# Kernel tuning notes

Measured on AMD Instinct MI355X. Metric: run time of the kernel, lower is better.

The kernel has to match this reference:

```python
import jax, jax.numpy as jnp
import numpy as np

B, NF, EMB = 2048, 32, 64
FEAT_MAP_DIM = [128, 128, 128]  # split_half=True, activation=None


def setup_inputs() -> dict:
    key = jax.random.key(0)
    ks = jax.random.split(key, 7)
    inp = jax.random.normal(ks[0], (B, NF, EMB), dtype=jnp.float32)
    # conv1d_i: in_channels = H_{i-1} * NF, out_channels = FEAT_MAP_DIM[i]
    # H_0 = NF = 32; H_1 = H_2 = 128 // 2 = 64 (split_half)
    in_chs = [NF * NF, (FEAT_MAP_DIM[0] // 2) * NF, (FEAT_MAP_DIM[1] // 2) * NF]
    params = {}
    for i, (ic, oc) in enumerate(zip(in_chs, FEAT_MAP_DIM)):
        bound = 1.0 / np.sqrt(ic)  # torch Conv1d default init range
        params[f"W{i}"] = jax.random.uniform(ks[1 + 2 * i], (oc, ic), jnp.float32, -bound, bound)
        params[f"b{i}"] = jax.random.uniform(ks[2 + 2 * i], (oc,), jnp.float32, -bound, bound)
    return {"inp": inp, **params}


def reference(inp, W0, b0, W1, b1, W2, b2):
    # CIN: h_k[b,o,e] = sum_{j,z} W_k[o, j*NF+z] * h_{k-1}[b,j,e] * inp[b,z,e] + b_k[o]
    # The torch code materializes the outer product then applies a 1x1 conv;
    # the fused triple einsum below computes identical math.
    nf = inp.shape[1]
    Ws, bs = [W0, W1, W2], [b0, b1, b2]
    h = inp
    outs = []
    n_layers = len(Ws)
    for i, (W, b) in enumerate(zip(Ws, bs)):
        O, Hj = W.shape[0], h.shape[1]
        Wr = W.reshape(O, Hj, nf)  # channel index c = j*nf + z
        nxt = jnp.einsum('bjk,bzk,ojz->bok', h, inp, Wr) + b[None, :, None]
        if i != n_layers - 1:  # split_half
            h, o = nxt[:, : O // 2], nxt[:, O // 2 :]
        else:
            o = nxt
        outs.append(o)
    out = jnp.concatenate(outs, axis=1)  # (B, 64+64+128, EMB)
    return jnp.sum(out, axis=2)  # (B, 256)
```

## Files before the change

### kernel.cpp

```cpp
#include <hip/hip_runtime.h>


typedef _Float16 f16;
typedef _Float16 f16x4 __attribute__((ext_vector_type(4)));
typedef _Float16 f16x8 __attribute__((ext_vector_type(8)));
typedef float f32x4 __attribute__((ext_vector_type(4)));
typedef float f32x16 __attribute__((ext_vector_type(16)));

#define HSTR 72
#define GSTR 163840
#define P0G  0
#define P1G  32768
#define P2G  98304

__device__ __forceinline__ f32x16 zero16() {
    f32x16 v;
#pragma unroll
    for (int i = 0; i < 16; ++i) v[i] = 0.0f;
    return v;
}

__global__ void __launch_bounds__(256)
prep_frag(const float* __restrict__ W0, const float* __restrict__ W1,
          const float* __restrict__ W2, f16* __restrict__ dst)
{
    int g = (blockIdx.x * 256 + threadIdx.x) * 8;
    const float* src; int base, KK, rbase;
    if (g < 65536)       { src = W0; base = 0;      KK = 64;  rbase = 0;  }
    else if (g < 131072) { src = W0; base = 65536;  KK = 64;  rbase = 64; }
    else if (g < 262144) { src = W1; base = 131072; KK = 128; rbase = 0;  }
    else if (g < 393216) { src = W1; base = 262144; KK = 128; rbase = 64; }
    else                 { src = W2; base = 393216; KK = 128; rbase = 0;  }
    int local = g - base;
    int frag  = local >> 9;
    int lane  = (local >> 3) & 63;
    int kk    = frag % KK;
    int mc    = frag / KK;
    int row   = rbase + mc * 32 + (lane & 31);
    int col   = kk * 16 + (lane >> 5) * 8;
    int IC    = KK * 16;
    const float* s = src + (size_t)row * IC + col;
    f16x8 o;
#pragma unroll
    for (int i = 0; i < 8; ++i) o[i] = (f16)s[i];
    *(f16x8*)(dst + g) = o;
}

__device__ __forceinline__ void p_chunk(const f16* __restrict__ hrows,
                                        const f16x8 (&pB)[4],
                                        f16* __restrict__ pdst, int jb,
                                        int t, int q)
{
    f32x16 acc = zero16();
#pragma unroll
    for (int s = 0; s < 4; ++s) {
        f16x8 a = *(const f16x8*)(hrows + t * HSTR + s * 16 + q * 8);
        acc = __builtin_amdgcn_mfma_f32_32x32x16_f16(a, pB[s], acc, 0, 0, 0);
    }
#pragma unroll
    for (int r = 0; r < 16; ++r) {
        int j = jb + (r & 3) + 8 * (r >> 2) + 4 * q;
        int f = j * 2 + (t >> 4);
        pdst[f * 512 + ((t >> 3) & 1) * 256 + (t & 7)] = (f16)acc[r];
    }
}

template <int HJ>
__device__ __forceinline__ void h_gemm4(const f16* __restrict__ Hf,
                                        const f16* __restrict__ h0,
                                        const f16* __restrict__ h1,
                                        int lane8, int t,
                                        const f16x8 (&ip)[2][2][2],
                                        f32x16 (&acc)[2][2])
{
    acc[0][0] = zero16(); acc[0][1] = zero16();
    acc[1][0] = zero16(); acc[1][1] = zero16();
    const f16* Wp = Hf + lane8;
    f16x8 wf[2][2];
    f16   sc[2][4];
#pragma unroll
    for (int ph = 0; ph < 2; ++ph) {
        wf[ph][0] = *(const f16x8*)(Wp + (ph * 2 + 0) * 512);
        wf[ph][1] = *(const f16x8*)(Wp + (ph * 2 + 1) * 512);
        sc[ph][0] = h0[ph * HSTR + t];
        sc[ph][1] = h0[ph * HSTR + 32 + t];
        sc[ph][2] = h1[ph * HSTR + t];
        sc[ph][3] = h1[ph * HSTR + 32 + t];
    }
    for (int jj = 0; jj < HJ; jj += 2) {
#pragma unroll
        for (int ph = 0; ph < 2; ++ph) {
            f16x8 w0 = wf[ph][0], w1 = wf[ph][1];
            f16 s00 = sc[ph][0], s01 = sc[ph][1];
            f16 s10 = sc[ph][2], s11 = sc[ph][3];
            int jn = jj + ph + 2;
            if (jn > HJ - 1) jn = HJ - 1;
            wf[ph][0] = *(const f16x8*)(Wp + (jn * 2 + 0) * 512);
            wf[ph][1] = *(const f16x8*)(Wp + (jn * 2 + 1) * 512);
            sc[ph][0] = h0[jn * HSTR + t];
            sc[ph][1] = h0[jn * HSTR + 32 + t];
            sc[ph][2] = h1[jn * HSTR + t];
            sc[ph][3] = h1[jn * HSTR + 32 + t];
            acc[0][0] = __builtin_amdgcn_mfma_f32_32x32x16_f16(w0, ip[0][0][0] * s00, acc[0][0], 0, 0, 0);
            acc[0][0] = __builtin_amdgcn_mfma_f32_32x32x16_f16(w1, ip[0][1][0] * s00, acc[0][0], 0, 0, 0);
            acc[0][1] = __builtin_amdgcn_mfma_f32_32x32x16_f16(w0, ip[0][0][1] * s01, acc[0][1], 0, 0, 0);
            acc[0][1] = __builtin_amdgcn_mfma_f32_32x32x16_f16(w1, ip[0][1][1] * s01, acc[0][1], 0, 0, 0);
            acc[1][0] = __builtin_amdgcn_mfma_f32_32x32x16_f16(w0, ip[1][0][0] * s10, acc[1][0], 0, 0, 0);
            acc[1][0] = __builtin_amdgcn_mfma_f32_32x32x16_f16(w1, ip[1][1][0] * s10, acc[1][0], 0, 0, 0);
            acc[1][1] = __builtin_amdgcn_mfma_f32_32x32x16_f16(w0, ip[1][0][1] * s11, acc[1][1], 0, 0, 0);
            acc[1][1] = __builtin_amdgcn_mfma_f32_32x32x16_f16(w1, ip[1][1][1] * s11, acc[1][1], 0, 0, 0);
        }
    }
}

__device__ __forceinline__ void load_bias(const float* __restrict__ bl,
                                          float (&bve)[16], int g, int q)
{
#pragma unroll
    for (int r = 0; r < 16; ++r)
        bve[r] = bl[g * 32 + (r & 3) + 8 * (r >> 2) + 4 * q];
}

__device__ __forceinline__ void epi4(const f32x16 (&acc)[2][2],
                                     f16* __restrict__ h0d, f16* __restrict__ h1d,
                                     const float (&bve)[16], int g, int t, int q)
{
#pragma unroll
    for (int r = 0; r < 16; ++r) {
        int row = g * 32 + (r & 3) + 8 * (r >> 2) + 4 * q;
        h0d[row * HSTR + t]      = (f16)(acc[0][0][r] + bve[r]);
        h0d[row * HSTR + 32 + t] = (f16)(acc[0][1][r] + bve[r]);
        h1d[row * HSTR + t]      = (f16)(acc[1][0][r] + bve[r]);
        h1d[row * HSTR + 32 + t] = (f16)(acc[1][1][r] + bve[r]);
    }
}

__global__ void __launch_bounds__(256, 2)
cin_h(const float* __restrict__ inp, const f16* __restrict__ Wf,
      f16* __restrict__ pW,
      const float* __restrict__ b0v, const float* __restrict__ b1v)
{
    __shared__ __attribute__((aligned(16))) f16 hL[4 * 64 * HSTR];

    const int tid   = threadIdx.x;
    const int w     = tid >> 6;
    const int lane  = tid & 63;
    const int t     = lane & 31;
    const int q     = lane >> 5;
    const int lane8 = lane * 8;
    const int bp    = w & 1;
    const int g     = w >> 1;
    const int b0i   = blockIdx.x * 4;

#pragma unroll
    for (int it = 0; it < 8; ++it) {
        int idx = it * 1024 + tid * 4;
        int b = idx >> 11, rem = idx & 2047;
        int z = rem >> 6, k = rem & 63;
        f32x4 v = *(const f32x4*)(inp + (size_t)(b0i + b) * 2048 + rem);
        f16x4 h4;
        h4[0] = (f16)v[0]; h4[1] = (f16)v[1]; h4[2] = (f16)v[2]; h4[3] = (f16)v[3];
        *(f16x4*)(hL + b * 64 * HSTR + z * HSTR + k) = h4;
    }
    __syncthreads();

    f16x8 ip[2][2][2];
#pragma unroll
    for (int b = 0; b < 2; ++b) {
        const f16* src = hL + (bp * 2 + b) * 64 * HSTR;
#pragma unroll
        for (int kq = 0; kq < 2; ++kq)
#pragma unroll
            for (int nh = 0; nh < 2; ++nh) {
                f16x8 v;
#pragma unroll
                for (int i = 0; i < 8; ++i)
                    v[i] = src[(kq * 16 + q * 8 + i) * HSTR + nh * 32 + t];
                ip[b][kq][nh] = v;
            }
    }
    f16x8 pB[4];
#pragma unroll
    for (int s = 0; s < 4; ++s)
        pB[s] = *(const f16x8*)(hL + w * 64 * HSTR + t * HSTR + s * 16 + q * 8);

    const int bglob = b0i + w;
    f16* pG = pW + (size_t)(bglob >> 5) * GSTR + (bglob & 31) * 8;
    const f16* H0 = Wf;
    const f16* H1 = Wf + 131072;
    f16* hA = hL + (bp * 2) * 64 * HSTR;
    f16* hB = hL + (bp * 2 + 1) * 64 * HSTR;
    f32x16 acc[2][2];
    float bve[16];

    p_chunk(hL + w * 64 * HSTR, pB, pG + P0G, 0, t, q);
    h_gemm4<32>(H0 + g * 64 * 512, hA, hB, lane8, t, ip, acc);
    load_bias(b0v, bve, g, q);
    __syncthreads();
    epi4(acc, hA, hB, bve, g, t, q);
    __syncthreads();

    p_chunk(hL + w * 64 * HSTR,             pB, pG + P1G, 0,  t, q);
    p_chunk(hL + w * 64 * HSTR + 32 * HSTR, pB, pG + P1G, 32, t, q);
    h_gemm4<64>(H1 + g * 128 * 512, hA, hB, lane8, t, ip, acc);
    load_bias(b1v, bve, g, q);
    __syncthreads();
    epi4(acc, hA, hB, bve, g, t, q);
    __syncthreads();

    p_chunk(hL + w * 64 * HSTR,             pB, pG + P2G, 0,  t, q);
    p_chunk(hL + w * 64 * HSTR + 32 * HSTR, pB, pG + P2G, 32, t, q);
}

template <int KK>
__device__ __forceinline__ void o_tile(const f16* __restrict__ Of,
                                       const f16* __restrict__ pBase,
                                       const float* __restrict__ biasp,
                                       float* __restrict__ out,
                                       float* __restrict__ rP,
                                       int bg, int colbase, int tid)
{
    const int w = tid >> 6, lane = tid & 63, t = lane & 31, q = lane >> 5;
    const int lane8 = lane * 8;
    const int mi = w & 1, ki = w >> 1;
    const int SQ = KK / 4;
    const f16* Ap = Of + (size_t)(mi * KK + ki * SQ) * 512 + lane8;
    const f16* Bp = pBase + (size_t)(ki * SQ) * 512 + lane8;

    f32x16 acc = zero16();
    f16x8 af[8], bf[8];
#pragma unroll
    for (int i = 0; i < 8; ++i) {
        af[i] = *(const f16x8*)(Ap + i * 512);
        bf[i] = *(const f16x8*)(Bp + i * 512);
    }
#pragma unroll 8
    for (int s = 0; s < SQ; ++s) {
        int idx = s & 7;
        f16x8 a = af[idx], b = bf[idx];
        int sn = s + 8 < SQ ? s + 8 : SQ - 1;
        af[idx] = *(const f16x8*)(Ap + sn * 512);
        bf[idx] = *(const f16x8*)(Bp + sn * 512);
        acc = __builtin_amdgcn_mfma_f32_32x32x16_f16(a, b, acc, 0, 0, 0);
    }
#pragma unroll
    for (int r = 0; r < 16; ++r) {
        int m = mi * 32 + (r & 3) + 8 * (r >> 2) + 4 * q;
        rP[(ki * 32 + t) * 64 + m] = acc[r];
    }
    __syncthreads();
    {
        int n = tid >> 4;
        int o = (tid & 15) * 4;
        f32x4 v = *(const f32x4*)(rP + n * 64 + o);
#pragma unroll
        for (int k2 = 1; k2 < 4; ++k2) {
            f32x4 u = *(const f32x4*)(rP + (k2 * 32 + n) * 64 + o);
            v[0] += u[0]; v[1] += u[1]; v[2] += u[2]; v[3] += u[3];
        }
        f32x4 bb = *(const f32x4*)(biasp + o);
        v[0] += 64.0f * bb[0]; v[1] += 64.0f * bb[1];
        v[2] += 64.0f * bb[2]; v[3] += 64.0f * bb[3];
        *(f32x4*)(out + (size_t)(bg * 32 + n) * 256 + colbase + o) = v;
    }
}

__global__ void __launch_bounds__(512, 2)
cin_out(const f16* __restrict__ Wf, const f16* __restrict__ pW,
        const float* __restrict__ b0v, const float* __restrict__ b1v,
        const float* __restrict__ b2v, float* __restrict__ out)
{
    __shared__ __attribute__((aligned(16))) float rP[4 * 32 * 64];
    const int tid = threadIdx.x;
    const int r  = blockIdx.x & 3;
    const int bg = blockIdx.x >> 2;
    const f16* pGrp = pW + (size_t)bg * GSTR;
    if (r == 0)
        o_tile<64> (Wf + 65536,  pGrp + P0G, b0v + 64, out, rP, bg, 0,   tid);
    else if (r == 1)
        o_tile<128>(Wf + 262144, pGrp + P1G, b1v + 64, out, rP, bg, 64,  tid);
    else if (r == 2)
        o_tile<128>(Wf + 393216, pGrp + P2G, b2v,      out, rP, bg, 128, tid);
    else
        o_tile<128>(Wf + 524288, pGrp + P2G, b2v + 64, out, rP, bg, 192, tid);
}

extern "C" void kernel_launch(void* const* d_in, const int* in_sizes, int n_in,
                              void* d_out, int out_size, void* d_ws, size_t ws_size,
                              hipStream_t stream)
{
    const float* inp = (const float*)d_in[0];
    const float* W0  = (const float*)d_in[1];
    const float* b0  = (const float*)d_in[2];
    const float* W1  = (const float*)d_in[3];
    const float* b1  = (const float*)d_in[4];
    const float* W2  = (const float*)d_in[5];
    const float* b2  = (const float*)d_in[6];
    float* out = (float*)d_out;

    f16* Wf = (f16*)d_ws;
    f16* pW = Wf + 655360;

    prep_frag<<<320, 256, 0, stream>>>(W0, W1, W2, Wf);
    cin_h<<<512, 256, 0, stream>>>(inp, Wf, pW, b0, b1);
    cin_out<<<256, 512, 0, stream>>>(Wf, pW, b0, b1, b2, out);
}
```

Baseline: 132.4 us.

## Process eight batch rows per cin_h block with four-batch register tiles

Each cin_h block now handles 8 batch elements instead of 4, and each wave computes a 64-row half of the H GEMM for 4 batches rather than 2. Every loaded W fragment therefore feeds twice as many MFMAs, halving W fragment traffic per batch. The cost is much higher register pressure (8 accumulators of 16 floats plus 16 input fragments), occupancy dropped to one block per CU, and half as many blocks (256), which risks spills and worse latency hiding.

After: 150.3 us. 13.5% more time.

```diff
diff --git a/kernel.cpp b/kernel.cpp
--- a/kernel.cpp
+++ b/kernel.cpp
@@ -66,49 +66,68 @@
 }
 
 template <int HJ>
-__device__ __forceinline__ void h_gemm4(const f16* __restrict__ Hf,
-                                        const f16* __restrict__ h0,
-                                        const f16* __restrict__ h1,
-                                        int lane8, int t,
-                                        const f16x8 (&ip)[2][2][2],
-                                        f32x16 (&acc)[2][2])
-{
-    acc[0][0] = zero16(); acc[0][1] = zero16();
-    acc[1][0] = zero16(); acc[1][1] = zero16();
+__device__ __forceinline__ void h_gemm_quad(const f16* __restrict__ Hf,
+                                            const f16* const (&hp)[4],
+                                            int lane8, int t,
+                                            const f16x8 (&ip)[4][2][2],
+                                            f32x16 (&acc)[4][2])
+{
+#pragma unroll
+    for (int b = 0; b < 4; ++b) { acc[b][0] = zero16(); acc[b][1] = zero16(); }
     const f16* Wp = Hf + lane8;
     f16x8 wf[2][2];
-    f16   sc[2][4];
+    f16   sc[2][4][2];
 #pragma unroll
     for (int ph = 0; ph < 2; ++ph) {
         wf[ph][0] = *(const f16x8*)(Wp + (ph * 2 + 0) * 512);
         wf[ph][1] = *(const f16x8*)(Wp + (ph * 2 + 1) * 512);
-        sc[ph][0] = h0[ph * HSTR + t];
-        sc[ph][1] = h0[ph * HSTR + 32 + t];
-        sc[ph][2] = h1[ph * HSTR + t];
-        sc[ph][3] = h1[ph * HSTR + 32 + t];
+#pragma unroll
+        for (int b = 0; b < 4; ++b) {
+            sc[ph][b][0] = hp[b][ph * HSTR + t];
+            sc[ph][b][1] = hp[b][ph * HSTR + 32 + t];
+        }
     }
     for (int jj = 0; jj < HJ; jj += 2) {
 #pragma unroll
         for (int ph = 0; ph < 2; ++ph) {
             f16x8 w0 = wf[ph][0], w1 = wf[ph][1];
-            f16 s00 = sc[ph][0], s01 = sc[ph][1];
-            f16 s10 = sc[ph][2], s11 = sc[ph][3];
+            f16 s[4][2];
+#pragma unroll
+            for (int b = 0; b < 4; ++b) {
+                s[b][0] = sc[ph][b][0];
+                s[b][1] = sc[ph][b][1];
+            }
             int jn = jj + ph + 2;
             if (jn > HJ - 1) jn = HJ - 1;
             wf[ph][0] = *(const f16x8*)(Wp + (jn * 2 + 0) * 512);
             wf[ph][1] = *(const f16x8*)(Wp + (jn * 2 + 1) * 512);
-            sc[ph][0] = h0[jn * HSTR + t];
-            sc[ph][1] = h0[jn * HSTR + 32 + t];
-            sc[ph][2] = h1[jn * HSTR + t];
-            sc[ph][3] = h1[jn * HSTR + 32 + t];
-            acc[0][0] = __builtin_amdgcn_mfma_f32_32x32x16_f16(w0, ip[0][0][0] * s00, acc[0][0], 0, 0, 0);
-            acc[0][0] = __builtin_amdgcn_mfma_f32_32x32x16_f16(w1, ip[0][1][0] * s00, acc[0][0], 0, 0, 0);
-            acc[0][1] = __builtin_amdgcn_mfma_f32_32x32x16_f16(w0, ip[0][0][1] * s01, acc[0][1], 0, 0, 0);
-            acc[0][1] = __builtin_amdgcn_mfma_f32_32x32x16_f16(w1, ip[0][1][1] * s01, acc[0][1], 0, 0, 0);
-            acc[1][0] = __builtin_amdgcn_mfma_f32_32x32x16_f16(w0, ip[1][0][0] * s10, acc[1][0], 0, 0, 0);
-            acc[1][0] = __builtin_amdgcn_mfma_f32_32x32x16_f16(w1, ip[1][1][0] * s10, acc[1][0], 0, 0, 0);
-            acc[1][1] = __builtin_amdgcn_mfma_f32_32x32x16_f16(w0, ip[1][0][1] * s11, acc[1][1], 0, 0, 0);
-            acc[1][1] = __builtin_amdgcn_mfma_f32_32x32x16_f16(w1, ip[1][1][1] * s11, acc[1][1], 0, 0, 0);
+#pragma unroll
+            for (int b = 0; b < 4; ++b) {
+                sc[ph][b][0] = hp[b][jn * HSTR + t];
+                sc[ph][b][1] = hp[b][jn * HSTR + 32 + t];
+            }
+            f16x8 pr0[4][2];
+#pragma unroll
+            for (int b = 0; b < 4; ++b) {
+                pr0[b][0] = ip[b][0][0] * s[b][0];
+                pr0[b][1] = ip[b][0][1] * s[b][1];
+            }
+#pragma unroll
+            for (int b = 0; b < 4; ++b) {
+                acc[b][0] = __builtin_amdgcn_mfma_f32_32x32x16_f16(w0, pr0[b][0], acc[b][0], 0, 0, 0);
+                acc[b][1] = __builtin_amdgcn_mfma_f32_32x32x16_f16(w0, pr0[b][1], acc[b][1], 0, 0, 0);
+            }
+            f16x8 pr1[4][2];
+#pragma unroll
+            for (int b = 0; b < 4; ++b) {
+                pr1[b][0] = ip[b][1][0] * s[b][0];
+                pr1[b][1] = ip[b][1][1] * s[b][1];
+            }
+#pragma unroll
+            for (int b = 0; b < 4; ++b) {
+                acc[b][0] = __builtin_amdgcn_mfma_f32_32x32x16_f16(w1, pr1[b][0], acc[b][0], 0, 0, 0);
+                acc[b][1] = __builtin_amdgcn_mfma_f32_32x32x16_f16(w1, pr1[b][1], acc[b][1], 0, 0, 0);
+            }
         }
     }
 }
@@ -121,26 +140,28 @@
         bve[r] = bl[g * 32 + (r & 3) + 8 * (r >> 2) + 4 * q];
 }
 
-__device__ __forceinline__ void epi4(const f32x16 (&acc)[2][2],
-                                     f16* __restrict__ h0d, f16* __restrict__ h1d,
-                                     const float (&bve)[16], int g, int t, int q)
+__device__ __forceinline__ void epi_quad(const f32x16 (&acc)[4][2],
+                                         f16* const (&hp)[4],
+                                         const float (&bve)[16],
+                                         int g, int t, int q)
 {
 #pragma unroll
     for (int r = 0; r < 16; ++r) {
         int row = g * 32 + (r & 3) + 8 * (r >> 2) + 4 * q;
-        h0d[row * HSTR + t]      = (f16)(acc[0][0][r] + bve[r]);
-        h0d[row * HSTR + 32 + t] = (f16)(acc[0][1][r] + bve[r]);
-        h1d[row * HSTR + t]      = (f16)(acc[1][0][r] + bve[r]);
-        h1d[row * HSTR + 32 + t] = (f16)(acc[1][1][r] + bve[r]);
-    }
-}
-
-__global__ void __launch_bounds__(256, 2)
+#pragma unroll
+        for (int b = 0; b < 4; ++b) {
+            hp[b][row * HSTR + t]      = (f16)(acc[b][0][r] + bve[r]);
+            hp[b][row * HSTR + 32 + t] = (f16)(acc[b][1][r] + bve[r]);
+        }
+    }
+}
+
+__global__ void __launch_bounds__(256, 1)
 cin_h(const float* __restrict__ inp, const f16* __restrict__ Wf,
       f16* __restrict__ pW,
       const float* __restrict__ b0v, const float* __restrict__ b1v)
 {
-    __shared__ __attribute__((aligned(16))) f16 hL[4 * 64 * HSTR];
+    __shared__ __attribute__((aligned(16))) f16 hL[8 * 64 * HSTR];
 
     const int tid   = threadIdx.x;
     const int w     = tid >> 6;
@@ -148,12 +169,12 @@
     const int t     = lane & 31;
     const int q     = lane >> 5;
     const int lane8 = lane * 8;
-    const int bp    = w & 1;
-    const int g     = w >> 1;
-    const int b0i   = blockIdx.x * 4;
-
-#pragma unroll
-    for (int it = 0; it < 8; ++it) {
+    const int g     = w & 1;
+    const int quad  = w >> 1;
+    const int b0i   = blockIdx.x * 8;
+
+#pragma unroll
+    for (int it = 0; it < 16; ++it) {
         int idx = it * 1024 + tid * 4;
         int b = idx >> 11, rem = idx & 2047;
         int z = rem >> 6, k = rem & 63;
@@ -164,10 +185,15 @@
     }
     __syncthreads();
 
-    f16x8 ip[2][2][2];
-#pragma unroll
-    for (int b = 0; b < 2; ++b) {
-        const f16* src = hL + (bp * 2 + b) * 64 * HSTR;
+    f16* hp[4];
+#pragma unroll
+    for (int b = 0; b < 4; ++b) hp[b] = hL + (quad * 4 + b) * 64 * HSTR;
+    const f16* const (&hpc)[4] = (const f16* const (&)[4])hp;
+
+    f16x8 ip[4][2][2];
+#pragma unroll
+    for (int b = 0; b < 4; ++b) {
+        const f16* src = hp[b];
 #pragma unroll
         for (int kq = 0; kq < 2; ++kq)
 #pragma unroll
@@ -179,37 +205,46 @@
                 ip[b][kq][nh] = v;
             }
     }
-    f16x8 pB[4];
-#pragma unroll
-    for (int s = 0; s < 4; ++s)
-        pB[s] = *(const f16x8*)(hL + w * 64 * HSTR + t * HSTR + s * 16 + q * 8);
-
-    const int bglob = b0i + w;
-    f16* pG = pW + (size_t)(bglob >> 5) * GSTR + (bglob & 31) * 8;
+    f16x8 pB[2][4];
+#pragma unroll
+    for (int lb = 0; lb < 2; ++lb)
+#pragma unroll
+        for (int s = 0; s < 4; ++s)
+            pB[lb][s] = *(const f16x8*)(hL + (w * 2 + lb) * 64 * HSTR +
+                                        t * HSTR + s * 16 + q * 8);
+    const f16* hq0 = hL + (w * 2) * 64 * HSTR;
+    const f16* hq1 = hL + (w * 2 + 1) * 64 * HSTR;
+    const int bg0 = b0i + w * 2, bg1 = b0i + w * 2 + 1;
+    f16* pG0 = pW + (size_t)(bg0 >> 5) * GSTR + (bg0 & 31) * 8;
+    f16* pG1 = pW + (size_t)(bg1 >> 5) * GSTR + (bg1 & 31) * 8;
+
     const f16* H0 = Wf;
     const f16* H1 = Wf + 131072;
-    f16* hA = hL + (bp * 2) * 64 * HSTR;
-    f16* hB = hL + (bp * 2 + 1) * 64 * HSTR;
-    f32x16 acc[2][2];
+    f32x16 acc[4][2];
     float bve[16];
 
-    p_chunk(hL + w * 64 * HSTR, pB, pG + P0G, 0, t, q);
-    h_gemm4<32>(H0 + g * 64 * 512, hA, hB, lane8, t, ip, acc);
+    p_chunk(hq0, pB[0], pG0 + P0G, 0, t, q);
+    p_chunk(hq1, pB[1], pG1 + P0G, 0, t, q);
+    h_gemm_quad<32>(H0 + g * 64 * 512, hpc, lane8, t, ip, acc);
     load_bias(b0v, bve, g, q);
     __syncthreads();
-    epi4(acc, hA, hB, bve, g, t, q);
-    __syncthreads();
-
-    p_chunk(hL + w * 64 * HSTR,             pB, pG + P1G, 0,  t, q);
-    p_chunk(hL + w * 64 * HSTR + 32 * HSTR, pB, pG + P1G, 32, t, q);
-    h_gemm4<64>(H1 + g * 128 * 512, hA, hB, lane8, t, ip, acc);
+    epi_quad(acc, hp, bve, g, t, q);
+    __syncthreads();
+
+    p_chunk(hq0,             pB[0], pG0 + P1G, 0,  t, q);
+    p_chunk(hq0 + 32 * HSTR, pB[0], pG0 + P1G, 32, t, q);
+    p_chunk(hq1,             pB[1], pG1 + P1G, 0,  t, q);
+    p_chunk(hq1 + 32 * HSTR, pB[1], pG1 + P1G, 32, t, q);
+    h_gemm_quad<64>(H1 + g * 128 * 512, hpc, lane8, t, ip, acc);
     load_bias(b1v, bve, g, q);
     __syncthreads();
-    epi4(acc, hA, hB, bve, g, t, q);
-    __syncthreads();
-
-    p_chunk(hL + w * 64 * HSTR,             pB, pG + P2G, 0,  t, q);
-    p_chunk(hL + w * 64 * HSTR + 32 * HSTR, pB, pG + P2G, 32, t, q);
+    epi_quad(acc, hp, bve, g, t, q);
+    __syncthreads();
+
+    p_chunk(hq0,             pB[0], pG0 + P2G, 0,  t, q);
+    p_chunk(hq0 + 32 * HSTR, pB[0], pG0 + P2G, 32, t, q);
+    p_chunk(hq1,             pB[1], pG1 + P2G, 0,  t, q);
+    p_chunk(hq1 + 32 * HSTR, pB[1], pG1 + P2G, 32, t, q);
 }
 
 template <int KK>
@@ -302,6 +337,6 @@
     f16* pW = Wf + 655360;
 
     prep_frag<<<320, 256, 0, stream>>>(W0, W1, W2, Wf);
-    cin_h<<<512, 256, 0, stream>>>(inp, Wf, pW, b0, b1);
+    cin_h<<<256, 256, 0, stream>>>(inp, Wf, pW, b0, b1);
     cin_out<<<256, 512, 0, stream>>>(Wf, pW, b0, b1, b2, out);
 }
```
